# Optimization experiments

Hardware: AMD Instinct MI355X
Metric: run time of the kernel (lower is better)

Reference implementation:

```python
import jax, jax.numpy as jnp
import numpy as np


def setup_inputs() -> dict:
    key = jax.random.key(0)
    ks = jax.random.split(key, 8)
    B, C, H, W = 8, 64, 256, 256
    Cq = C // 8
    return {
        "x": jax.random.normal(ks[0], (B, C, H, W), dtype=jnp.float32),
        "Wq": jax.random.normal(ks[1], (Cq, C), dtype=jnp.float32) * 0.1,
        "bq": jax.random.normal(ks[2], (Cq,), dtype=jnp.float32) * 0.1,
        "Wk": jax.random.normal(ks[3], (Cq, C), dtype=jnp.float32) * 0.1,
        "bk": jax.random.normal(ks[4], (Cq,), dtype=jnp.float32) * 0.1,
        "Wv": jax.random.normal(ks[5], (C, C), dtype=jnp.float32) * 0.1,
        "bv": jax.random.normal(ks[6], (C,), dtype=jnp.float32) * 0.1,
        "gamma": jax.random.normal(ks[7], (1,), dtype=jnp.float32),
    }


def _criss_cross(x, Wq, bq, Wk, bk, Wv, bv, gamma):
    # 1x1 convs == per-pixel linear maps over channel dim
    q = jnp.einsum('bchw,oc->bohw', x, Wq) + bq[None, :, None, None]  # [B,Cq,H,W]
    k = jnp.einsum('bchw,oc->bohw', x, Wk) + bk[None, :, None, None]  # [B,Cq,H,W]
    v = jnp.einsum('bchw,oc->bohw', x, Wv) + bv[None, :, None, None]  # [B,C,H,W]

    # --- column (height) attention: independent per (b, w) ---
    # attn_h[b,w,i,j] = <q[:, :, i, w], k[:, :, j, w]>, softmax over j
    attn_h = jnp.einsum('bciw,bcjw->bwij', q, k)            # [B,W,H,H]
    attn_h = jax.nn.softmax(attn_h, axis=-1)
    # torch: h_out = bmm(value[BW,C,H], attn[BW,H,H]) -> out[c,j] = sum_i v[c,i]*attn[i,j]
    h_out = jnp.einsum('bciw,bwij->bcjw', v, attn_h)        # [B,C,H,W]

    # --- row (width) attention: independent per (b, h) ---
    attn_w = jnp.einsum('bchw,bchv->bhwv', q, k)            # [B,H,W,W]
    attn_w = jax.nn.softmax(attn_w, axis=-1)
    w_out = jnp.einsum('bchw,bhwv->bchv', v, attn_w)        # [B,C,H,W]

    return gamma[0] * (h_out + w_out) + x


def reference(x, Wq, bq, Wk, bk, Wv, bv, gamma):
    return _criss_cross(x, Wq, bq, Wk, bk, Wv, bv, gamma)
```

## Files before the change

kernel.cpp:

```cpp
#include <hip/hip_runtime.h>
#include <cstddef>

namespace {

constexpr int    Bn   = 8;
constexpr int    Cc   = 64;
constexpr int    Cq   = 8;
constexpr int    Ln   = 256;
constexpr size_t HWn  = 65536;
constexpr size_t NPIX = (size_t)Bn * HWn;
constexpr size_t VPLANE = NPIX * 16;

constexpr float LOG2E = 1.44269504088896f;

constexpr size_t WT_B = 0;
constexpr size_t QH_B = 32768;
constexpr size_t QL_B = QH_B + NPIX * 8 * 2;
constexpr size_t KH_B = QL_B + NPIX * 8 * 2;
constexpr size_t KL_B = KH_B + NPIX * 8 * 2;
constexpr size_t VB_B = KL_B + NPIX * 8 * 2;
constexpr size_t HO_B = VB_B + NPIX * 64 * 2;
constexpr size_t WO_B = HO_B + NPIX * 64 * 2;

typedef short bf16x8 __attribute__((ext_vector_type(8)));
typedef float f32x16 __attribute__((ext_vector_type(16)));
typedef unsigned short u16x4 __attribute__((ext_vector_type(4)));

__device__ __forceinline__ float bf2f(unsigned short h) {
  union { unsigned u; float f; } c; c.u = ((unsigned)h) << 16;
  return c.f;
}
__device__ __forceinline__ float fbits(unsigned u) {
  union { unsigned u; float f; } c; c.u = u; return c.f;
}
__device__ __forceinline__ unsigned cvt_pk_bf16(float a, float b) {
  unsigned r;
  asm("v_cvt_pk_bf16_f32 %0, %1, %2" : "=v"(r) : "v"(a), "v"(b));
  return r;
}
__device__ __forceinline__ float fast_exp2(float x) {
#if __has_builtin(__builtin_amdgcn_exp2f)
  return __builtin_amdgcn_exp2f(x);
#else
  float r;
  asm("v_exp_f32 %0, %1" : "=v"(r) : "v"(x));
  return r;
#endif
}
__device__ __forceinline__ f32x16 zero16() {
  f32x16 z;
#pragma unroll
  for (int i = 0; i < 16; ++i) z[i] = 0.f;
  return z;
}

}

__global__ void pack_weights(const float* __restrict__ Wq,
                             const float* __restrict__ Wk,
                             const float* __restrict__ Wv,
                             float* __restrict__ wt) {
  int idx = blockIdx.x * 256 + threadIdx.x;
  if (idx >= 64 * 80) return;
  int c = idx / 80, o = idx % 80;
  float v;
  if (o < 8)       v = Wq[o * 64 + c] * LOG2E;
  else if (o < 16) v = Wk[(o - 8) * 64 + c];
  else             v = Wv[(o - 16) * 64 + c];
  wt[idx] = v;
}

__global__ __launch_bounds__(256) void qkv_kernel(
    const float* __restrict__ x, const float* __restrict__ wt,
    const float* __restrict__ bq, const float* __restrict__ bk,
    const float* __restrict__ bv,
    unsigned short* __restrict__ qh, unsigned short* __restrict__ ql,
    unsigned short* __restrict__ kh, unsigned short* __restrict__ kl,
    unsigned short* __restrict__ vb) {
  const int d = blockIdx.x;
  const int lin = (d & 7) * 1280 + (d >> 3);
  const int chunk = lin % 5;
  size_t p = (size_t)(lin / 5) * 256 + threadIdx.x;
  int b = (int)(p >> 16);
  int rem = (int)(p & 65535);
  const float* xbase = x + (size_t)b * 64 * HWn + rem;

  float acc[16];
  if (chunk == 0) {
#pragma unroll
    for (int o = 0; o < 8; ++o) { acc[o] = bq[o] * LOG2E; acc[8 + o] = bk[o]; }
  } else {
#pragma unroll
    for (int o = 0; o < 16; ++o) acc[o] = bv[(chunk - 1) * 16 + o];
  }
  const int woff = (chunk == 0) ? 0 : 16 + (chunk - 1) * 16;

  float xa[8], xn[8];
#pragma unroll
  for (int cc = 0; cc < 8; ++cc) xa[cc] = xbase[(size_t)cc * HWn];

#pragma unroll 1
  for (int c0 = 0; c0 < 64; c0 += 16) {
#pragma unroll
    for (int cc = 0; cc < 8; ++cc) xn[cc] = xbase[(size_t)(c0 + 8 + cc) * HWn];
#pragma unroll
    for (int cc = 0; cc < 8; ++cc) {
      const float* w = wt + (c0 + cc) * 80 + woff;
      const float xc = xa[cc];
#pragma unroll
      for (int o = 0; o < 16; ++o) acc[o] = fmaf(xc, w[o], acc[o]);
    }
    const int cnx = (c0 + 16) & 63;
#pragma unroll
    for (int cc = 0; cc < 8; ++cc) xa[cc] = xbase[(size_t)(cnx + cc) * HWn];
#pragma unroll
    for (int cc = 0; cc < 8; ++cc) {
      const float* w = wt + (c0 + 8 + cc) * 80 + woff;
      const float xc = xn[cc];
#pragma unroll
      for (int o = 0; o < 16; ++o) acc[o] = fmaf(xc, w[o], acc[o]);
    }
  }

  if (chunk == 0) {
    unsigned dh[8], dl[8];
#pragma unroll
    for (int k = 0; k < 8; ++k) {
      float a0 = acc[2 * k], a1 = acc[2 * k + 1];
      unsigned h = cvt_pk_bf16(a0, a1);
      dl[k] = cvt_pk_bf16(a0 - fbits(h << 16), a1 - fbits(h & 0xffff0000u));
      dh[k] = h;
    }
    *(uint4*)(qh + p * 8) = make_uint4(dh[0], dh[1], dh[2], dh[3]);
    *(uint4*)(ql + p * 8) = make_uint4(dl[0], dl[1], dl[2], dl[3]);
    *(uint4*)(kh + p * 8) = make_uint4(dh[4], dh[5], dh[6], dh[7]);
    *(uint4*)(kl + p * 8) = make_uint4(dl[4], dl[5], dl[6], dl[7]);
  } else {
    unsigned dv[8];
#pragma unroll
    for (int k = 0; k < 8; ++k) dv[k] = cvt_pk_bf16(acc[2 * k], acc[2 * k + 1]);
    unsigned short* vp = vb + (size_t)(chunk - 1) * VPLANE + p * 16;
    *(uint4*)(vp + 0) = make_uint4(dv[0], dv[1], dv[2], dv[3]);
    *(uint4*)(vp + 8) = make_uint4(dv[4], dv[5], dv[6], dv[7]);
  }
}

template <int MODE>
__global__ __launch_bounds__(256) void attn_kernel(
    const unsigned short* __restrict__ qh, const unsigned short* __restrict__ ql,
    const unsigned short* __restrict__ kh, const unsigned short* __restrict__ kl,
    const unsigned short* __restrict__ vb, _Float16* __restrict__ o) {
  const int s = (MODE == 1) ? (((blockIdx.x & 7) << 8) | (blockIdx.x >> 3))
                            : blockIdx.x;
  const int t = threadIdx.x;
  const int b = s >> 8;
  const int r = s & 255;
  const int w = t >> 6;
  const int l = t & 63;
  const int g = l >> 5;
  const int ln = l & 31;

  __shared__ short qs_h[256 * 8], qs_l[256 * 8];
  __shared__ short ks_h[256 * 8], ks_l[256 * 8];
  __shared__ short vz[16384];
  __shared__ float Zl[256];

  float* Zp = (float*)vz;

  size_t qkb, qk_stride;
  size_t v_pix_base, v_pix_stride;
  if (MODE == 0) {
    qkb    = (size_t)s * (Ln * Cq);  qk_stride = Cq;
    v_pix_base = (size_t)s * Ln;     v_pix_stride = 1;
  } else {
    qkb    = ((size_t)b * HWn + r) * Cq;  qk_stride = (size_t)Ln * Cq;
    v_pix_base = (size_t)b * HWn + r;     v_pix_stride = Ln;
  }

  const int rem_i = t >> 4;
  const int c4 = (t & 15) << 2;
  const int a_ = rem_i >> 3, g2 = (rem_i >> 2) & 1, t0 = rem_i & 3;
  const int e_ = 4 * a_ + t0;
  const int mt_ = c4 >> 5;
  const int lane_s0 = 32 * g2 + (c4 & 31);
  short* vz0 = &vz[(mt_ * 64 + lane_s0) * 8 + e_];
  const unsigned short* vp0 = vb + (size_t)(c4 >> 4) * VPLANE +
                              (v_pix_base + (size_t)rem_i * v_pix_stride) * 16 +
                              (c4 & 15);
  const size_t step = (size_t)256 * v_pix_stride;

  {
    const size_t off = qkb + (size_t)t * qk_stride;
    *(bf16x8*)&qs_h[t * 8] = *(const bf16x8*)(qh + off);
    *(bf16x8*)&qs_l[t * 8] = *(const bf16x8*)(ql + off);
    *(bf16x8*)&ks_h[t * 8] = *(const bf16x8*)(kh + off);
    *(bf16x8*)&ks_l[t * 8] = *(const bf16x8*)(kl + off);
  }
  u16x4 raw_pre[16];
#pragma unroll
  for (int rnd = 0; rnd < 16; ++rnd)
    raw_pre[rnd] = *(const u16x4*)(vp0 + rnd * step);
  __syncthreads();

  {
    const short* kb = g ? ks_l : ks_h;
    const int wg = (w << 1) | g;
    bf16x8 afk0 = *(const bf16x8*)&kb[(ln + 32 * (2 * w + 0)) * 8];
    bf16x8 afk1 = *(const bf16x8*)&kb[(ln + 32 * (2 * w + 1)) * 8];
#pragma unroll 1
    for (int it = 0; it < 8; ++it) {
      int i = ln + 32 * it;
      bf16x8 bh = *(const bf16x8*)&qs_h[i * 8];
      bf16x8 bl = *(const bf16x8*)&qs_l[i * 8];
      float z0 = 0.f, z1 = 0.f, z2 = 0.f, z3 = 0.f;
      {
        f32x16 c = zero16();
        c = __builtin_amdgcn_mfma_f32_32x32x16_bf16(afk0, bh, c, 0, 0, 0);
        c = __builtin_amdgcn_mfma_f32_32x32x16_bf16(afk0, bl, c, 0, 0, 0);
#pragma unroll
        for (int rr = 0; rr < 16; ++rr) {
          float e = fast_exp2(c[rr]);
          if ((rr & 3) == 0) z0 += e; else if ((rr & 3) == 1) z1 += e;
          else if ((rr & 3) == 2) z2 += e; else z3 += e;
        }
      }
      {
        f32x16 c = zero16();
        c = __builtin_amdgcn_mfma_f32_32x32x16_bf16(afk1, bh, c, 0, 0, 0);
        c = __builtin_amdgcn_mfma_f32_32x32x16_bf16(afk1, bl, c, 0, 0, 0);
#pragma unroll
        for (int rr = 0; rr < 16; ++rr) {
          float e = fast_exp2(c[rr]);
          if ((rr & 3) == 0) z0 += e; else if ((rr & 3) == 1) z1 += e;
          else if ((rr & 3) == 2) z2 += e; else z3 += e;
        }
      }
      Zp[(wg << 8) + i] = (z0 + z1) + (z2 + z3);
    }
  }
  __syncthreads();
  {
    float z = 0.f;
#pragma unroll
    for (int k = 0; k < 8; ++k) z += Zp[(k << 8) + t];
    Zl[t] = 1.0f / z;
  }
  __syncthreads();

#pragma unroll
  for (int rnd = 0; rnd < 16; ++rnd) {
    float iz = Zl[(rnd << 4) + rem_i];
#pragma unroll
    for (int u = 0; u < 4; ++u) {
      unsigned dd = cvt_pk_bf16(bf2f(raw_pre[rnd][u]) * iz, 0.f);
      vz0[rnd * 1024 + u * 8] = (short)dd;
    }
  }
  __syncthreads();

  f32x16 acc00 = zero16(), acc01 = zero16(), acc10 = zero16(), acc11 = zero16();
  {
    bf16x8 bkh[2], bkl[2];
#pragma unroll
    for (int nt2 = 0; nt2 < 2; ++nt2) {
      int j = ln + 32 * (2 * w + nt2);
      bkh[nt2] = *(const bf16x8*)&ks_h[j * 8];
      bkl[nt2] = *(const bf16x8*)&ks_l[j * 8];
    }
    const short* qb = g ? qs_l : qs_h;
#pragma unroll 1
    for (int it = 0; it < 8; ++it) {
      int i = ln + 32 * it;
      bf16x8 aQ = *(const bf16x8*)&qb[i * 8];
      bf16x8 pf[2][2];
#pragma unroll
      for (int nt2 = 0; nt2 < 2; ++nt2) {
        f32x16 c = zero16();
        c = __builtin_amdgcn_mfma_f32_32x32x16_bf16(aQ, bkh[nt2], c, 0, 0, 0);
        c = __builtin_amdgcn_mfma_f32_32x32x16_bf16(aQ, bkl[nt2], c, 0, 0, 0);
        union { unsigned u[4]; bf16x8 v; } cv0, cv1;
#pragma unroll
        for (int k = 0; k < 4; ++k)
          cv0.u[k] = cvt_pk_bf16(fast_exp2(c[2 * k]), fast_exp2(c[2 * k + 1]));
#pragma unroll
        for (int k = 0; k < 4; ++k)
          cv1.u[k] = cvt_pk_bf16(fast_exp2(c[8 + 2 * k]), fast_exp2(c[8 + 2 * k + 1]));
        pf[nt2][0] = cv0.v;
        pf[nt2][1] = cv1.v;
      }
#pragma unroll
      for (int s2 = 0; s2 < 2; ++s2) {
#pragma unroll
        for (int mt = 0; mt < 2; ++mt) {
          bf16x8 vf = *(const bf16x8*)&vz[(((it * 2 + s2) * 2 + mt) * 64 + l) * 8];
          if (mt == 0) {
            acc00 = __builtin_amdgcn_mfma_f32_32x32x16_bf16(vf, pf[0][s2], acc00, 0, 0, 0);
            acc10 = __builtin_amdgcn_mfma_f32_32x32x16_bf16(vf, pf[1][s2], acc10, 0, 0, 0);
          } else {
            acc01 = __builtin_amdgcn_mfma_f32_32x32x16_bf16(vf, pf[0][s2], acc01, 0, 0, 0);
            acc11 = __builtin_amdgcn_mfma_f32_32x32x16_bf16(vf, pf[1][s2], acc11, 0, 0, 0);
          }
        }
      }
    }
  }

#pragma unroll
  for (int nt2 = 0; nt2 < 2; ++nt2) {
    int j = ln + 32 * (2 * w + nt2);
#pragma unroll
    for (int mt = 0; mt < 2; ++mt) {
      const f32x16& A = (nt2 == 0) ? (mt == 0 ? acc00 : acc01)
                                   : (mt == 0 ? acc10 : acc11);
#pragma unroll
      for (int reg = 0; reg < 16; ++reg) {
        int c = (reg & 3) + 8 * (reg >> 2) + 4 * g + 32 * mt;
        if (MODE == 0) {
          o[((size_t)b * 64 + c) * HWn + (size_t)r * 256 + j] = (_Float16)A[reg];
        } else {
          o[((size_t)s * 64 + c) * 256 + j] = (_Float16)A[reg];
        }
      }
    }
  }
}

__global__ __launch_bounds__(256) void merge_kernel(
    const _Float16* __restrict__ wo, const _Float16* __restrict__ ho,
    const float* __restrict__ x, const float* __restrict__ gamma,
    float* __restrict__ out) {
  const int h0 = blockIdx.x * 64;
  const int c = blockIdx.y;
  const int b = blockIdx.z;
  const int t = threadIdx.x;
  __shared__ _Float16 lds[256 * 66];

  const float g = gamma[0];

#pragma unroll
  for (int it = 0; it < 8; ++it) {
    int e = it * 256 + t;
    int w = e >> 3, q8 = (e & 7) << 3;
    uint4 f = *(const uint4*)&ho[(((size_t)b * 256 + w) * 64 + c) * 256 + h0 + q8];
    unsigned* dst = (unsigned*)&lds[w * 66 + q8];
    dst[0] = f.x; dst[1] = f.y; dst[2] = f.z; dst[3] = f.w;
  }
  __syncthreads();

#pragma unroll 4
  for (int rr = 0; rr < 64; ++rr) {
    size_t idx = (((size_t)b * 64 + c) * 256 + h0 + rr) * 256 + t;
    out[idx] = g * ((float)wo[idx] + (float)lds[t * 66 + rr]) + x[idx];
  }
}

extern "C" void kernel_launch(void* const* d_in, const int* in_sizes, int n_in,
                              void* d_out, int out_size, void* d_ws, size_t ws_size,
                              hipStream_t stream) {
  const float* x     = (const float*)d_in[0];
  const float* Wq    = (const float*)d_in[1];
  const float* bq    = (const float*)d_in[2];
  const float* Wk    = (const float*)d_in[3];
  const float* bk    = (const float*)d_in[4];
  const float* Wv    = (const float*)d_in[5];
  const float* bv    = (const float*)d_in[6];
  const float* gamma = (const float*)d_in[7];
  float* out = (float*)d_out;
  char*  ws  = (char*)d_ws;

  float*          wt = (float*)(ws + WT_B);
  unsigned short* qh = (unsigned short*)(ws + QH_B);
  unsigned short* ql = (unsigned short*)(ws + QL_B);
  unsigned short* kh = (unsigned short*)(ws + KH_B);
  unsigned short* kl = (unsigned short*)(ws + KL_B);
  unsigned short* vb = (unsigned short*)(ws + VB_B);
  _Float16*       ho = (_Float16*)(ws + HO_B);
  _Float16*       wo = (_Float16*)(ws + WO_B);

  hipLaunchKernelGGL(pack_weights, dim3(20), dim3(256), 0, stream, Wq, Wk, Wv, wt);
  hipLaunchKernelGGL(qkv_kernel, dim3(10240), dim3(256), 0, stream,
                     x, wt, bq, bk, bv, qh, ql, kh, kl, vb);
  hipLaunchKernelGGL((attn_kernel<0>), dim3(2048), dim3(256), 0, stream,
                     qh, ql, kh, kl, vb, wo);
  hipLaunchKernelGGL((attn_kernel<1>), dim3(2048), dim3(256), 0, stream,
                     qh, ql, kh, kl, vb, ho);
  hipLaunchKernelGGL(merge_kernel, dim3(4, 64, 8), dim3(256), 0, stream,
                     wo, ho, x, gamma, out);
}
```

Before: 466.7 us.

## Halve attention V staging buffer and split QKV projection into separate Q/K and V kernels

```diff
diff --git a/kernel.cpp b/kernel.cpp
--- a/kernel.cpp
+++ b/kernel.cpp
@@ -70,30 +70,76 @@
   wt[idx] = v;
 }
 
-__global__ __launch_bounds__(256) void qkv_kernel(
+__global__ __launch_bounds__(256) void qk_kernel(
     const float* __restrict__ x, const float* __restrict__ wt,
     const float* __restrict__ bq, const float* __restrict__ bk,
-    const float* __restrict__ bv,
     unsigned short* __restrict__ qh, unsigned short* __restrict__ ql,
-    unsigned short* __restrict__ kh, unsigned short* __restrict__ kl,
-    unsigned short* __restrict__ vb) {
-  const int d = blockIdx.x;
-  const int lin = (d & 7) * 1280 + (d >> 3);
-  const int chunk = lin % 5;
-  size_t p = (size_t)(lin / 5) * 256 + threadIdx.x;
+    unsigned short* __restrict__ kh, unsigned short* __restrict__ kl) {
+  size_t p = (size_t)blockIdx.x * 256 + threadIdx.x;
   int b = (int)(p >> 16);
   int rem = (int)(p & 65535);
   const float* xbase = x + (size_t)b * 64 * HWn + rem;
 
   float acc[16];
-  if (chunk == 0) {
-#pragma unroll
-    for (int o = 0; o < 8; ++o) { acc[o] = bq[o] * LOG2E; acc[8 + o] = bk[o]; }
-  } else {
-#pragma unroll
-    for (int o = 0; o < 16; ++o) acc[o] = bv[(chunk - 1) * 16 + o];
-  }
-  const int woff = (chunk == 0) ? 0 : 16 + (chunk - 1) * 16;
+#pragma unroll
+  for (int o = 0; o < 8; ++o) { acc[o] = bq[o] * LOG2E; acc[8 + o] = bk[o]; }
+
+  float xa[8], xn[8];
+#pragma unroll
+  for (int cc = 0; cc < 8; ++cc) xa[cc] = xbase[(size_t)cc * HWn];
+
+#pragma unroll 1
+  for (int c0 = 0; c0 < 64; c0 += 16) {
+#pragma unroll
+    for (int cc = 0; cc < 8; ++cc) xn[cc] = xbase[(size_t)(c0 + 8 + cc) * HWn];
+#pragma unroll
+    for (int cc = 0; cc < 8; ++cc) {
+      const float* w = wt + (c0 + cc) * 80;
+      const float xc = xa[cc];
+#pragma unroll
+      for (int o = 0; o < 16; ++o) acc[o] = fmaf(xc, w[o], acc[o]);
+    }
+    const int cnx = (c0 + 16) & 63;
+#pragma unroll
+    for (int cc = 0; cc < 8; ++cc) xa[cc] = xbase[(size_t)(cnx + cc) * HWn];
+#pragma unroll
+    for (int cc = 0; cc < 8; ++cc) {
+      const float* w = wt + (c0 + 8 + cc) * 80;
+      const float xc = xn[cc];
+#pragma unroll
+      for (int o = 0; o < 16; ++o) acc[o] = fmaf(xc, w[o], acc[o]);
+    }
+  }
+
+  unsigned dh[8], dl[8];
+#pragma unroll
+  for (int k = 0; k < 8; ++k) {
+    float a0 = acc[2 * k], a1 = acc[2 * k + 1];
+    unsigned h = cvt_pk_bf16(a0, a1);
+    dl[k] = cvt_pk_bf16(a0 - fbits(h << 16), a1 - fbits(h & 0xffff0000u));
+    dh[k] = h;
+  }
+  *(uint4*)(qh + p * 8) = make_uint4(dh[0], dh[1], dh[2], dh[3]);
+  *(uint4*)(ql + p * 8) = make_uint4(dl[0], dl[1], dl[2], dl[3]);
+  *(uint4*)(kh + p * 8) = make_uint4(dh[4], dh[5], dh[6], dh[7]);
+  *(uint4*)(kl + p * 8) = make_uint4(dl[4], dl[5], dl[6], dl[7]);
+}
+
+__global__ __launch_bounds__(256) void v_kernel(
+    const float* __restrict__ x, const float* __restrict__ wt,
+    const float* __restrict__ bv, unsigned short* __restrict__ vb) {
+  const int d = blockIdx.x;
+  const int lin = (d & 7) * 1024 + (d >> 3);
+  const int chunk = lin & 3;
+  size_t p = (size_t)(lin >> 2) * 256 + threadIdx.x;
+  int b = (int)(p >> 16);
+  int rem = (int)(p & 65535);
+  const float* xbase = x + (size_t)b * 64 * HWn + rem;
+
+  float acc[16];
+#pragma unroll
+  for (int o = 0; o < 16; ++o) acc[o] = bv[chunk * 16 + o];
+  const int woff = 16 + chunk * 16;
 
   float xa[8], xn[8];
 #pragma unroll
@@ -122,27 +168,12 @@
     }
   }
 
-  if (chunk == 0) {
-    unsigned dh[8], dl[8];
-#pragma unroll
-    for (int k = 0; k < 8; ++k) {
-      float a0 = acc[2 * k], a1 = acc[2 * k + 1];
-      unsigned h = cvt_pk_bf16(a0, a1);
-      dl[k] = cvt_pk_bf16(a0 - fbits(h << 16), a1 - fbits(h & 0xffff0000u));
-      dh[k] = h;
-    }
-    *(uint4*)(qh + p * 8) = make_uint4(dh[0], dh[1], dh[2], dh[3]);
-    *(uint4*)(ql + p * 8) = make_uint4(dl[0], dl[1], dl[2], dl[3]);
-    *(uint4*)(kh + p * 8) = make_uint4(dh[4], dh[5], dh[6], dh[7]);
-    *(uint4*)(kl + p * 8) = make_uint4(dl[4], dl[5], dl[6], dl[7]);
-  } else {
-    unsigned dv[8];
-#pragma unroll
-    for (int k = 0; k < 8; ++k) dv[k] = cvt_pk_bf16(acc[2 * k], acc[2 * k + 1]);
-    unsigned short* vp = vb + (size_t)(chunk - 1) * VPLANE + p * 16;
-    *(uint4*)(vp + 0) = make_uint4(dv[0], dv[1], dv[2], dv[3]);
-    *(uint4*)(vp + 8) = make_uint4(dv[4], dv[5], dv[6], dv[7]);
-  }
+  unsigned dv[8];
+#pragma unroll
+  for (int k = 0; k < 8; ++k) dv[k] = cvt_pk_bf16(acc[2 * k], acc[2 * k + 1]);
+  unsigned short* vp = vb + (size_t)chunk * VPLANE + p * 16;
+  *(uint4*)(vp + 0) = make_uint4(dv[0], dv[1], dv[2], dv[3]);
+  *(uint4*)(vp + 8) = make_uint4(dv[4], dv[5], dv[6], dv[7]);
 }
 
 template <int MODE>
@@ -162,7 +193,7 @@
 
   __shared__ short qs_h[256 * 8], qs_l[256 * 8];
   __shared__ short ks_h[256 * 8], ks_l[256 * 8];
-  __shared__ short vz[16384];
+  __shared__ short vz[8192];
   __shared__ float Zl[256];
 
   float* Zp = (float*)vz;
@@ -196,9 +227,9 @@
     *(bf16x8*)&ks_h[t * 8] = *(const bf16x8*)(kh + off);
     *(bf16x8*)&ks_l[t * 8] = *(const bf16x8*)(kl + off);
   }
-  u16x4 raw_pre[16];
-#pragma unroll
-  for (int rnd = 0; rnd < 16; ++rnd)
+  u16x4 raw_pre[8];
+#pragma unroll
+  for (int rnd = 0; rnd < 8; ++rnd)
     raw_pre[rnd] = *(const u16x4*)(vp0 + rnd * step);
   __syncthreads();
 
@@ -248,7 +279,7 @@
   __syncthreads();
 
 #pragma unroll
-  for (int rnd = 0; rnd < 16; ++rnd) {
+  for (int rnd = 0; rnd < 8; ++rnd) {
     float iz = Zl[(rnd << 4) + rem_i];
 #pragma unroll
     for (int u = 0; u < 4; ++u) {
@@ -256,20 +287,26 @@
       vz0[rnd * 1024 + u * 8] = (short)dd;
     }
   }
+  u16x4 raw2[8];
+#pragma unroll
+  for (int rnd = 0; rnd < 8; ++rnd)
+    raw2[rnd] = *(const u16x4*)(vp0 + (8 + rnd) * step);
   __syncthreads();
 
   f32x16 acc00 = zero16(), acc01 = zero16(), acc10 = zero16(), acc11 = zero16();
-  {
-    bf16x8 bkh[2], bkl[2];
-#pragma unroll
-    for (int nt2 = 0; nt2 < 2; ++nt2) {
-      int j = ln + 32 * (2 * w + nt2);
-      bkh[nt2] = *(const bf16x8*)&ks_h[j * 8];
-      bkl[nt2] = *(const bf16x8*)&ks_l[j * 8];
-    }
-    const short* qb = g ? qs_l : qs_h;
+  bf16x8 bkh[2], bkl[2];
+#pragma unroll
+  for (int nt2 = 0; nt2 < 2; ++nt2) {
+    int j = ln + 32 * (2 * w + nt2);
+    bkh[nt2] = *(const bf16x8*)&ks_h[j * 8];
+    bkl[nt2] = *(const bf16x8*)&ks_l[j * 8];
+  }
+  const short* qb = g ? qs_l : qs_h;
+
+#pragma unroll
+  for (int half = 0; half < 2; ++half) {
 #pragma unroll 1
-    for (int it = 0; it < 8; ++it) {
+    for (int it = half * 4; it < half * 4 + 4; ++it) {
       int i = ln + 32 * it;
       bf16x8 aQ = *(const bf16x8*)&qb[i * 8];
       bf16x8 pf[2][2];
@@ -292,7 +329,7 @@
       for (int s2 = 0; s2 < 2; ++s2) {
 #pragma unroll
         for (int mt = 0; mt < 2; ++mt) {
-          bf16x8 vf = *(const bf16x8*)&vz[(((it * 2 + s2) * 2 + mt) * 64 + l) * 8];
+          bf16x8 vf = *(const bf16x8*)&vz[((((it & 3) * 2 + s2) * 2 + mt) * 64 + l) * 8];
           if (mt == 0) {
             acc00 = __builtin_amdgcn_mfma_f32_32x32x16_bf16(vf, pf[0][s2], acc00, 0, 0, 0);
             acc10 = __builtin_amdgcn_mfma_f32_32x32x16_bf16(vf, pf[1][s2], acc10, 0, 0, 0);
@@ -302,6 +339,19 @@
           }
         }
       }
+    }
+    if (half == 0) {
+      __syncthreads();
+#pragma unroll
+      for (int rnd = 0; rnd < 8; ++rnd) {
+        float iz = Zl[((rnd + 8) << 4) + rem_i];
+#pragma unroll
+        for (int u = 0; u < 4; ++u) {
+          unsigned dd = cvt_pk_bf16(bf2f(raw2[rnd][u]) * iz, 0.f);
+          vz0[rnd * 1024 + u * 8] = (short)dd;
+        }
+      }
+      __syncthreads();
     }
   }
 
@@ -378,8 +428,10 @@
   _Float16*       wo = (_Float16*)(ws + WO_B);
 
   hipLaunchKernelGGL(pack_weights, dim3(20), dim3(256), 0, stream, Wq, Wk, Wv, wt);
-  hipLaunchKernelGGL(qkv_kernel, dim3(10240), dim3(256), 0, stream,
-                     x, wt, bq, bk, bv, qh, ql, kh, kl, vb);
+  hipLaunchKernelGGL(qk_kernel, dim3(2048), dim3(256), 0, stream,
+                     x, wt, bq, bk, qh, ql, kh, kl);
+  hipLaunchKernelGGL(v_kernel, dim3(8192), dim3(256), 0, stream,
+                     x, wt, bv, vb);
   hipLaunchKernelGGL((attn_kernel<0>), dim3(2048), dim3(256), 0, stream,
                      qh, ql, kh, kl, vb, wo);
   hipLaunchKernelGGL((attn_kernel<1>), dim3(2048), dim3(256), 0, stream,
```

New measurement: 479.6 us. 2.8% more time.

## Halve V LDS staging, swizzle LDS layout, merge both attention modes into one launch

Applied to the files above, without the earlier changes.

```diff
diff --git a/kernel.cpp b/kernel.cpp
--- a/kernel.cpp
+++ b/kernel.cpp
@@ -145,13 +145,16 @@
   }
 }
 
-template <int MODE>
 __global__ __launch_bounds__(256) void attn_kernel(
     const unsigned short* __restrict__ qh, const unsigned short* __restrict__ ql,
     const unsigned short* __restrict__ kh, const unsigned short* __restrict__ kl,
-    const unsigned short* __restrict__ vb, _Float16* __restrict__ o) {
-  const int s = (MODE == 1) ? (((blockIdx.x & 7) << 8) | (blockIdx.x >> 3))
-                            : blockIdx.x;
+    const unsigned short* __restrict__ vb,
+    _Float16* __restrict__ wo, _Float16* __restrict__ ho) {
+  const int bid = blockIdx.x;
+  const int mode = bid >> 11;
+  const int inner = bid & 2047;
+  const int s = mode ? (((inner & 7) << 8) | (inner >> 3)) : inner;
+  _Float16* o = mode ? ho : wo;
   const int t = threadIdx.x;
   const int b = s >> 8;
   const int r = s & 255;
@@ -162,14 +165,14 @@
 
   __shared__ short qs_h[256 * 8], qs_l[256 * 8];
   __shared__ short ks_h[256 * 8], ks_l[256 * 8];
-  __shared__ short vz[16384];
+  __shared__ short vz[8192];
   __shared__ float Zl[256];
 
   float* Zp = (float*)vz;
 
   size_t qkb, qk_stride;
   size_t v_pix_base, v_pix_stride;
-  if (MODE == 0) {
+  if (mode == 0) {
     qkb    = (size_t)s * (Ln * Cq);  qk_stride = Cq;
     v_pix_base = (size_t)s * Ln;     v_pix_stride = 1;
   } else {
@@ -183,11 +186,14 @@
   const int e_ = 4 * a_ + t0;
   const int mt_ = c4 >> 5;
   const int lane_s0 = 32 * g2 + (c4 & 31);
-  short* vz0 = &vz[(mt_ * 64 + lane_s0) * 8 + e_];
+  const unsigned key_w = (unsigned)((g2 << 2) | ((t & 7) >> 1));
+  const unsigned wbase = ((unsigned)(((mt_ * 64 + lane_s0) * 8 + e_) * 2)) ^ (key_w << 4);
+  char* vzb = (char*)vz;
   const unsigned short* vp0 = vb + (size_t)(c4 >> 4) * VPLANE +
                               (v_pix_base + (size_t)rem_i * v_pix_stride) * 16 +
                               (c4 & 15);
   const size_t step = (size_t)256 * v_pix_stride;
+  const int lsw = l ^ ((l >> 3) & 7);
 
   {
     const size_t off = qkb + (size_t)t * qk_stride;
@@ -196,9 +202,9 @@
     *(bf16x8*)&ks_h[t * 8] = *(const bf16x8*)(kh + off);
     *(bf16x8*)&ks_l[t * 8] = *(const bf16x8*)(kl + off);
   }
-  u16x4 raw_pre[16];
-#pragma unroll
-  for (int rnd = 0; rnd < 16; ++rnd)
+  u16x4 raw_pre[8];
+#pragma unroll
+  for (int rnd = 0; rnd < 8; ++rnd)
     raw_pre[rnd] = *(const u16x4*)(vp0 + rnd * step);
   __syncthreads();
 
@@ -248,28 +254,34 @@
   __syncthreads();
 
 #pragma unroll
-  for (int rnd = 0; rnd < 16; ++rnd) {
+  for (int rnd = 0; rnd < 8; ++rnd) {
     float iz = Zl[(rnd << 4) + rem_i];
 #pragma unroll
     for (int u = 0; u < 4; ++u) {
       unsigned dd = cvt_pk_bf16(bf2f(raw_pre[rnd][u]) * iz, 0.f);
-      vz0[rnd * 1024 + u * 8] = (short)dd;
-    }
-  }
+      *(short*)(vzb + ((wbase ^ (unsigned)(u << 4)) + rnd * 2048)) = (short)dd;
+    }
+  }
+  u16x4 raw2[8];
+#pragma unroll
+  for (int rnd = 0; rnd < 8; ++rnd)
+    raw2[rnd] = *(const u16x4*)(vp0 + (8 + rnd) * step);
   __syncthreads();
 
   f32x16 acc00 = zero16(), acc01 = zero16(), acc10 = zero16(), acc11 = zero16();
-  {
-    bf16x8 bkh[2], bkl[2];
-#pragma unroll
-    for (int nt2 = 0; nt2 < 2; ++nt2) {
-      int j = ln + 32 * (2 * w + nt2);
-      bkh[nt2] = *(const bf16x8*)&ks_h[j * 8];
-      bkl[nt2] = *(const bf16x8*)&ks_l[j * 8];
-    }
-    const short* qb = g ? qs_l : qs_h;
+  bf16x8 bkh[2], bkl[2];
+#pragma unroll
+  for (int nt2 = 0; nt2 < 2; ++nt2) {
+    int j = ln + 32 * (2 * w + nt2);
+    bkh[nt2] = *(const bf16x8*)&ks_h[j * 8];
+    bkl[nt2] = *(const bf16x8*)&ks_l[j * 8];
+  }
+  const short* qb = g ? qs_l : qs_h;
+
+#pragma unroll
+  for (int half = 0; half < 2; ++half) {
 #pragma unroll 1
-    for (int it = 0; it < 8; ++it) {
+    for (int it = half * 4; it < half * 4 + 4; ++it) {
       int i = ln + 32 * it;
       bf16x8 aQ = *(const bf16x8*)&qb[i * 8];
       bf16x8 pf[2][2];
@@ -292,7 +304,7 @@
       for (int s2 = 0; s2 < 2; ++s2) {
 #pragma unroll
         for (int mt = 0; mt < 2; ++mt) {
-          bf16x8 vf = *(const bf16x8*)&vz[(((it * 2 + s2) * 2 + mt) * 64 + l) * 8];
+          bf16x8 vf = *(const bf16x8*)&vz[((((it & 3) * 2 + s2) * 2 + mt) * 64 + lsw) * 8];
           if (mt == 0) {
             acc00 = __builtin_amdgcn_mfma_f32_32x32x16_bf16(vf, pf[0][s2], acc00, 0, 0, 0);
             acc10 = __builtin_amdgcn_mfma_f32_32x32x16_bf16(vf, pf[1][s2], acc10, 0, 0, 0);
@@ -303,6 +315,19 @@
         }
       }
     }
+    if (half == 0) {
+      __syncthreads();
+#pragma unroll
+      for (int rnd = 0; rnd < 8; ++rnd) {
+        float iz = Zl[((rnd + 8) << 4) + rem_i];
+#pragma unroll
+        for (int u = 0; u < 4; ++u) {
+          unsigned dd = cvt_pk_bf16(bf2f(raw2[rnd][u]) * iz, 0.f);
+          *(short*)(vzb + ((wbase ^ (unsigned)(u << 4)) + rnd * 2048)) = (short)dd;
+        }
+      }
+      __syncthreads();
+    }
   }
 
 #pragma unroll
@@ -315,7 +340,7 @@
 #pragma unroll
       for (int reg = 0; reg < 16; ++reg) {
         int c = (reg & 3) + 8 * (reg >> 2) + 4 * g + 32 * mt;
-        if (MODE == 0) {
+        if (mode == 0) {
           o[((size_t)b * 64 + c) * HWn + (size_t)r * 256 + j] = (_Float16)A[reg];
         } else {
           o[((size_t)s * 64 + c) * 256 + j] = (_Float16)A[reg];
@@ -380,10 +405,8 @@
   hipLaunchKernelGGL(pack_weights, dim3(20), dim3(256), 0, stream, Wq, Wk, Wv, wt);
   hipLaunchKernelGGL(qkv_kernel, dim3(10240), dim3(256), 0, stream,
                      x, wt, bq, bk, bv, qh, ql, kh, kl, vb);
-  hipLaunchKernelGGL((attn_kernel<0>), dim3(2048), dim3(256), 0, stream,
-                     qh, ql, kh, kl, vb, wo);
-  hipLaunchKernelGGL((attn_kernel<1>), dim3(2048), dim3(256), 0, stream,
-                     qh, ql, kh, kl, vb, ho);
+  hipLaunchKernelGGL(attn_kernel, dim3(4096), dim3(256), 0, stream,
+                     qh, ql, kh, kl, vb, wo, ho);
   hipLaunchKernelGGL(merge_kernel, dim3(4, 64, 8), dim3(256), 0, stream,
                      wo, ho, x, gamma, out);
 }
```

Result: faster. 451.7 us (-3.2%).
